# Kernel tuning notes

Measured on AMD Instinct MI355X. Metric: run time of the kernel, lower is better.

## Reference

```python
import jax, jax.numpy as jnp
import numpy as np

B, S, D, H = 4, 2048, 1024, 16
DK = D // H

def setup_inputs() -> dict:
    key = jax.random.key(0)
    ks = jax.random.split(key, 12)
    s = 1.0 / np.sqrt(D)
    return {
        "query": jax.random.normal(ks[0], (B, S, D), jnp.float32),
        "key": jax.random.normal(ks[1], (B, S, D), jnp.float32),
        "value": jax.random.normal(ks[2], (B, S, D), jnp.float32),
        "mask": jax.random.randint(ks[3], (B, S, S), 0, 2, jnp.int32),
        "Wq": jax.random.normal(ks[4], (D, D), jnp.float32) * s,
        "bq": jnp.zeros((D,), jnp.float32),
        "Wk": jax.random.normal(ks[5], (D, D), jnp.float32) * s,
        "bk": jnp.zeros((D,), jnp.float32),
        "Wv": jax.random.normal(ks[6], (D, D), jnp.float32) * s,
        "bv": jnp.zeros((D,), jnp.float32),
        "Wo": jax.random.normal(ks[7], (D, D), jnp.float32) * s,
        "bo": jnp.zeros((D,), jnp.float32),
    }

def _split_heads(x):
    b, s, _ = x.shape
    return x.reshape(b, s, H, DK).transpose(0, 2, 1, 3)  # [b,h,s,dk]

def reference(query, key, value, mask, Wq, bq, Wk, bk, Wv, bv, Wo, bo):
    # torch nn.Linear: y = x @ W.T + b
    Q = _split_heads(query @ Wq.T + bq)
    K = _split_heads(key @ Wk.T + bk)
    V = _split_heads(value @ Wv.T + bv)
    scores = jnp.einsum('bhqd,bhkd->bhqk', Q, K) / np.sqrt(DK)
    scores = jnp.where(mask[:, None, :, :] == 0, jnp.float32(-1e9), scores)
    probs = jax.nn.softmax(scores, axis=-1)
    attn = jnp.einsum('bhqk,bhkd->bhqd', probs, V)
    out = attn.transpose(0, 2, 1, 3).reshape(query.shape[0], -1, H * DK)
    return out @ Wo.T + bo
```

## Files before the change

kernel.cpp:

```cpp
#include <hip/hip_runtime.h>

typedef __attribute__((ext_vector_type(8))) short short8;
typedef __attribute__((ext_vector_type(8))) unsigned short ushort8_t;
typedef __attribute__((ext_vector_type(4))) float floatx4;
typedef __attribute__((ext_vector_type(2))) _Float16 half2_t;
typedef __attribute__((ext_vector_type(4))) _Float16 half4;
typedef __attribute__((ext_vector_type(8))) _Float16 half8;

#define B_ 4
#define S_ 2048
#define D_ 1024
#define H_ 16
#define DK_ 64
#define BS_ (B_ * S_)

union V8u { half8 v8; half4 v4[2]; };
union H16 { _Float16 h; unsigned short u; };

typedef const __attribute__((address_space(1))) void* gvp;
typedef __attribute__((address_space(3))) void* lvp;

static __device__ __forceinline__ unsigned short f2bf(float f) {
  union { float f; unsigned int u; } x; x.f = f;
  unsigned int r = x.u + 0x7fffu + ((x.u >> 16) & 1u);
  return (unsigned short)(r >> 16);
}

static __device__ __forceinline__ half2_t pk_f16(float a, float b) {
  return __builtin_bit_cast(half2_t, __builtin_amdgcn_cvt_pkrtz(a, b));
}

__global__ void cast_kernel(const float* __restrict__ in, unsigned short* __restrict__ out, int n4) {
  int i = blockIdx.x * blockDim.x + threadIdx.x;
  if (i < n4) {
    float4 v = ((const float4*)in)[i];
    ushort4 o;
    o.x = f2bf(v.x); o.y = f2bf(v.y); o.z = f2bf(v.z); o.w = f2bf(v.w);
    ((ushort4*)out)[i] = o;
  }
}

__global__ void cast4_kernel(const float* __restrict__ a, const float* __restrict__ b,
                             const float* __restrict__ c, const float* __restrict__ d,
                             unsigned short* __restrict__ oa, unsigned short* __restrict__ ob,
                             unsigned short* __restrict__ oc, unsigned short* __restrict__ od, int n4) {
  int i = blockIdx.x * blockDim.x + threadIdx.x;
  int w = blockIdx.y;
  const float* src = (w == 0) ? a : (w == 1) ? b : (w == 2) ? c : d;
  unsigned short* dst = (w == 0) ? oa : (w == 1) ? ob : (w == 2) ? oc : od;
  if (i < n4) {
    float4 v = ((const float4*)src)[i];
    ushort4 o;
    o.x = f2bf(v.x); o.y = f2bf(v.y); o.z = f2bf(v.z); o.w = f2bf(v.w);
    ((ushort4*)dst)[i] = o;
  }
}

__global__ void pack_mask(const int* __restrict__ mask, unsigned long long* __restrict__ bits) {
  int i = blockIdx.x * blockDim.x + threadIdx.x;
  unsigned long long m = __ballot(mask[i] != 0);
  if ((threadIdx.x & 63) == 0) bits[i >> 6] = m;
}

__global__ void transpose_v(const unsigned short* __restrict__ Vh, unsigned short* __restrict__ Vt) {
  __shared__ unsigned short T[64][72];
  int bh = blockIdx.y;
  int s0 = blockIdx.x * 64;
  int tid = threadIdx.x;
  int r = tid >> 3, c = (tid & 7) * 8;
  const unsigned short* src = Vh + ((size_t)bh * S_ + s0) * DK_;
#pragma unroll
  for (int p = 0; p < 2; ++p)
    *(uint4*)(&T[r + p * 32][c]) = *(const uint4*)(src + (size_t)(r + p * 32) * DK_ + c);
  __syncthreads();
  unsigned short* dst = Vt + (size_t)bh * DK_ * S_;
#pragma unroll
  for (int p = 0; p < 2; ++p) {
    int d = r + p * 32;
    ushort8_t o;
#pragma unroll
    for (int i = 0; i < 8; ++i) {
      int pos = c + i;
      int th = pos >> 5, rem = pos & 31;
      int q4 = rem >> 3, rem2 = rem & 7;
      int t = th * 2 + (rem2 >> 2), j = rem2 & 3;
      int k = t * 16 + q4 * 4 + j;
      o[i] = T[k][d];
    }
    *(ushort8_t*)(dst + (size_t)d * S_ + s0 + c) = o;
  }
}

__global__ __launch_bounds__(256) void gemm_bt(
    const unsigned short* __restrict__ X,
    const unsigned short* __restrict__ W,
    const float* __restrict__ bias,
    void* __restrict__ Y, int M, int N, int K, float scale, int mode)
{
  __shared__ __align__(16) unsigned short As[128 * 64];
  __shared__ __align__(16) unsigned short Bs[128 * 64];
  int tid = threadIdx.x;
  int wave = tid >> 6, lane = tid & 63, quad = lane >> 4, li = lane & 15;
  int wm = wave >> 1, wn = wave & 1;
  int bm = blockIdx.y, bn = blockIdx.x;

  int srow = lane >> 3;
  int scol = ((lane & 7) ^ srow) * 8;
  const unsigned short* gA = X + (size_t)(bm * 128 + wave * 32 + srow) * K + scol;
  const unsigned short* gB = W + (size_t)(bn * 128 + wave * 32 + srow) * K + scol;
  unsigned short* ldsA = &As[wave * 2048];
  unsigned short* ldsB = &Bs[wave * 2048];

  floatx4 acc[4][4] = {};

  for (int k0 = 0; k0 < K; k0 += 64) {
    __syncthreads();
#pragma unroll
    for (int j = 0; j < 4; ++j) {
      __builtin_amdgcn_global_load_lds((gvp)(gA + (size_t)(j * 8) * K + k0), (lvp)(ldsA + j * 512), 16, 0, 0);
      __builtin_amdgcn_global_load_lds((gvp)(gB + (size_t)(j * 8) * K + k0), (lvp)(ldsB + j * 512), 16, 0, 0);
    }
    __syncthreads();
#pragma unroll
    for (int s2 = 0; s2 < 2; ++s2) {
      short8 af[4], bf[4];
#pragma unroll
      for (int t = 0; t < 4; ++t) {
        int ra = wm * 64 + t * 16 + li;
        int rb = wn * 64 + t * 16 + li;
        int slot = ((s2 * 4 + quad) ^ (li & 7)) * 8;
        af[t] = *(const short8*)(&As[ra * 64 + slot]);
        bf[t] = *(const short8*)(&Bs[rb * 64 + slot]);
      }
#pragma unroll
      for (int mt = 0; mt < 4; ++mt)
#pragma unroll
        for (int nt = 0; nt < 4; ++nt)
          acc[mt][nt] = __builtin_amdgcn_mfma_f32_16x16x32_bf16(af[mt], bf[nt], acc[mt][nt], 0, 0, 0);
    }
  }

#pragma unroll
  for (int nt = 0; nt < 4; ++nt) {
    int n = bn * 128 + wn * 64 + nt * 16 + li;
    float bv = bias[n];
#pragma unroll
    for (int mt = 0; mt < 4; ++mt) {
#pragma unroll
      for (int r = 0; r < 4; ++r) {
        int m = bm * 128 + wm * 64 + mt * 16 + quad * 4 + r;
        float v = (acc[mt][nt][r] + bv) * scale;
        if (mode == 1) {
          ((float*)Y)[(size_t)m * N + n] = v;
        } else {
          int b = m >> 11, s = m & 2047, h = n >> 6, dk = n & 63;
          size_t idx = (((size_t)(b * H_ + h)) * S_ + s) * DK_ + dk;
          if (mode == 0) {
            ((unsigned short*)Y)[idx] = f2bf(v);
          } else {
            H16 hv; hv.h = (_Float16)v;
            ((unsigned short*)Y)[idx] = hv.u;
          }
        }
      }
    }
  }
}

__global__ __launch_bounds__(256) void attn_kernel(
    const unsigned short* __restrict__ Qh,
    const unsigned short* __restrict__ Kh,
    const _Float16* __restrict__ Vt,
    const unsigned long long* __restrict__ mbits,
    unsigned short* __restrict__ attnb)
{
  __shared__ __align__(16) unsigned short Ks[64 * 64];
  __shared__ __align__(16) unsigned short Vs[64 * 64];

  int tid = threadIdx.x;
  int wave = tid >> 6, lane = tid & 63, quad = lane >> 4, li = lane & 15;

  int blk = blockIdx.x;
  int xcd = blk & 7, slot7 = blk >> 3;
  int bh = xcd * 8 + (slot7 >> 4);
  int qb = slot7 & 15;
  int b = bh >> 4, h = bh & 15;
  int qbase = qb * 128 + wave * 32;
  const size_t hq = (size_t)bh * S_ * DK_;

  short8 aQ[2][2];
#pragma unroll
  for (int qs = 0; qs < 2; ++qs)
#pragma unroll
    for (int s2 = 0; s2 < 2; ++s2)
      aQ[qs][s2] = *(const short8*)(Qh + hq + (size_t)(qbase + qs * 16 + li) * DK_ + s2 * 32 + quad * 8);

  floatx4 o[2][4] = {};
  float l[2] = {0.f, 0.f};

  const unsigned long long* mrow = mbits + ((size_t)b * S_ + qbase + li) * (S_ / 64);

  int srow = lane >> 3;
  int scol = ((lane & 7) ^ srow) * 8;
  const unsigned short* gK = Kh + hq + (size_t)(wave * 16 + srow) * DK_ + scol;
  const _Float16* gV = Vt + ((size_t)bh * 64 + wave * 16 + srow) * S_ + scol;
  unsigned short* ldsK = &Ks[(wave * 16) * 64];
  unsigned short* ldsV = &Vs[(wave * 16) * 64];

  for (int k0 = 0; k0 < S_; k0 += 64) {
    int kw = k0 >> 6;
    __syncthreads();
#pragma unroll
    for (int j = 0; j < 2; ++j) {
      __builtin_amdgcn_global_load_lds((gvp)(gK + (size_t)(k0 + j * 8) * DK_), (lvp)(ldsK + j * 512), 16, 0, 0);
      __builtin_amdgcn_global_load_lds((gvp)(gV + (size_t)(j * 8) * S_ + k0), (lvp)(ldsV + j * 512), 16, 0, 0);
    }
    unsigned long long mw0 = mrow[kw];
    unsigned long long mw1 = mrow[16 * (S_ / 64) + kw];
    __syncthreads();

    short8 bK[4][2];
#pragma unroll
    for (int t = 0; t < 4; ++t)
#pragma unroll
      for (int s2 = 0; s2 < 2; ++s2)
        bK[t][s2] = *(const short8*)(&Ks[(t * 16 + li) * 64 + (((s2 * 4 + quad) ^ (li & 7)) * 8)]);

    floatx4 sc[4][2] = {};
#pragma unroll
    for (int s2 = 0; s2 < 2; ++s2)
#pragma unroll
      for (int t = 0; t < 4; ++t)
#pragma unroll
        for (int qs = 0; qs < 2; ++qs)
          sc[t][qs] = __builtin_amdgcn_mfma_f32_16x16x32_bf16(bK[t][s2], aQ[qs][s2], sc[t][qs], 0, 0, 0);

    unsigned long long sh0 = mw0 >> (quad * 4);
    unsigned long long sh1 = mw1 >> (quad * 4);

    half4 aP[4][2];
#pragma unroll
    for (int t = 0; t < 4; ++t)
#pragma unroll
      for (int qs = 0; qs < 2; ++qs) {
        unsigned nb = (unsigned)(((qs ? sh1 : sh0) >> (t * 16)) & 15u);
        float p0 = (nb & 1u)        ? exp2f(sc[t][qs][0]) : 0.f;
        float p1 = ((nb >> 1) & 1u) ? exp2f(sc[t][qs][1]) : 0.f;
        float p2 = ((nb >> 2) & 1u) ? exp2f(sc[t][qs][2]) : 0.f;
        float p3 = ((nb >> 3) & 1u) ? exp2f(sc[t][qs][3]) : 0.f;
        l[qs] += (p0 + p1) + (p2 + p3);
        half2_t plo = pk_f16(p0, p1);
        half2_t phi = pk_f16(p2, p3);
        aP[t][qs] = __builtin_shufflevector(plo, phi, 0, 1, 2, 3);
      }

    V8u vv[4][2];
#pragma unroll
    for (int dt = 0; dt < 4; ++dt)
#pragma unroll
      for (int tp = 0; tp < 2; ++tp)
        vv[dt][tp].v8 = *(const half8*)((const _Float16*)&Vs[(dt * 16 + li) * 64 + (((tp * 4 + quad) ^ (li & 7)) * 8)]);

#pragma unroll
    for (int t = 0; t < 4; ++t)
#pragma unroll
      for (int qs = 0; qs < 2; ++qs)
#pragma unroll
        for (int dt = 0; dt < 4; ++dt)
          o[qs][dt] = __builtin_amdgcn_mfma_f32_16x16x16f16(aP[t][qs], vv[dt][t >> 1].v4[t & 1], o[qs][dt], 0, 0, 0);
  }

  float inv[2];
#pragma unroll
  for (int qs = 0; qs < 2; ++qs) {
    float lf = l[qs];
    lf += __shfl_xor(lf, 16, 64);
    lf += __shfl_xor(lf, 32, 64);
    inv[qs] = 1.0f / lf;
  }
#pragma unroll
  for (int qs = 0; qs < 2; ++qs)
#pragma unroll
    for (int r = 0; r < 4; ++r) {
      float ir = __shfl(inv[qs], quad * 4 + r, 64);
      size_t row = (size_t)b * S_ + qbase + qs * 16 + quad * 4 + r;
#pragma unroll
      for (int dt = 0; dt < 4; ++dt)
        attnb[row * D_ + h * DK_ + dt * 16 + li] = f2bf(o[qs][dt][r] * ir);
    }
}

extern "C" void kernel_launch(void* const* d_in, const int* in_sizes, int n_in,
                              void* d_out, int out_size, void* d_ws, size_t ws_size,
                              hipStream_t stream) {
  const float* query = (const float*)d_in[0];
  const float* key   = (const float*)d_in[1];
  const float* value = (const float*)d_in[2];
  const int*   mask  = (const int*)d_in[3];
  const float* Wq = (const float*)d_in[4];
  const float* bq = (const float*)d_in[5];
  const float* Wk = (const float*)d_in[6];
  const float* bk = (const float*)d_in[7];
  const float* Wv = (const float*)d_in[8];
  const float* bv = (const float*)d_in[9];
  const float* Wo = (const float*)d_in[10];
  const float* bo = (const float*)d_in[11];
  float* out = (float*)d_out;

  char* ws = (char*)d_ws;
  size_t off = 0;
  auto alloc = [&](size_t bytes) -> void* {
    void* p = ws + off;
    off += (bytes + 255) & ~(size_t)255;
    return p;
  };
  unsigned short* Xb    = (unsigned short*)alloc((size_t)BS_ * D_ * 2);
  unsigned short* Wqb   = (unsigned short*)alloc((size_t)D_ * D_ * 2);
  unsigned short* Wkb   = (unsigned short*)alloc((size_t)D_ * D_ * 2);
  unsigned short* Wvb   = (unsigned short*)alloc((size_t)D_ * D_ * 2);
  unsigned short* Wob   = (unsigned short*)alloc((size_t)D_ * D_ * 2);
  unsigned short* Qh    = (unsigned short*)alloc((size_t)BS_ * D_ * 2);
  unsigned short* Kh    = (unsigned short*)alloc((size_t)BS_ * D_ * 2);
  unsigned short* Vh    = (unsigned short*)alloc((size_t)BS_ * D_ * 2);
  unsigned short* Vt    = (unsigned short*)alloc((size_t)BS_ * D_ * 2);
  unsigned short* attnb = (unsigned short*)alloc((size_t)BS_ * D_ * 2);
  unsigned long long* mbits = (unsigned long long*)alloc((size_t)B_ * S_ * (S_ / 64) * 8);

  const float SC = 0.18033688011112042f;

  pack_mask<<<(B_ * S_ * S_) / 256, 256, 0, stream>>>(mask, mbits);

  int wn4 = D_ * D_ / 4;
  cast4_kernel<<<dim3(wn4 / 256, 4), 256, 0, stream>>>(Wq, Wk, Wv, Wo, Wqb, Wkb, Wvb, Wob, wn4);

  int xn4 = BS_ * D_ / 4;
  dim3 gg(D_ / 128, BS_ / 128), gb(256);

  cast_kernel<<<xn4 / 256, 256, 0, stream>>>(query, Xb, xn4);
  gemm_bt<<<gg, gb, 0, stream>>>(Xb, Wqb, bq, Qh, BS_, D_, D_, SC, 0);
  cast_kernel<<<xn4 / 256, 256, 0, stream>>>(key, Xb, xn4);
  gemm_bt<<<gg, gb, 0, stream>>>(Xb, Wkb, bk, Kh, BS_, D_, D_, 1.0f, 0);
  cast_kernel<<<xn4 / 256, 256, 0, stream>>>(value, Xb, xn4);
  gemm_bt<<<gg, gb, 0, stream>>>(Xb, Wvb, bv, Vh, BS_, D_, D_, 1.0f, 2);
  transpose_v<<<dim3(S_ / 64, B_ * H_), 256, 0, stream>>>(Vh, Vt);

  attn_kernel<<<dim3(8 * 8 * 16), 256, 0, stream>>>(Qh, Kh, (const _Float16*)Vt, mbits, attnb);

  gemm_bt<<<gg, gb, 0, stream>>>(attnb, Wob, bo, out, BS_, D_, D_, 1.0f, 1);
}
```

Baseline: 503.4 us.

## Double-buffer GEMM and attention LDS tiles, batch QKV casts and projections

Adds double-buffered shared-memory staging to both the GEMM core and the attention kernel, so the next K/V or A/B tile is prefetched while the current one feeds MFMA, with one barrier per iteration instead of two. The mask words for the next tile are also prefetched. The three input casts and the three QKV projections are merged into single launches over a z-dimension, using separate bf16 buffers. This doubles LDS usage per block, which may reduce occupancy, and uses more workspace memory.

```diff
diff --git a/kernel.cpp b/kernel.cpp
--- a/kernel.cpp
+++ b/kernel.cpp
@@ -30,13 +30,19 @@
   return __builtin_bit_cast(half2_t, __builtin_amdgcn_cvt_pkrtz(a, b));
 }
 
-__global__ void cast_kernel(const float* __restrict__ in, unsigned short* __restrict__ out, int n4) {
+__global__ void cast3_kernel(const float* __restrict__ a, const float* __restrict__ b,
+                             const float* __restrict__ c,
+                             unsigned short* __restrict__ oa, unsigned short* __restrict__ ob,
+                             unsigned short* __restrict__ oc, int n4) {
   int i = blockIdx.x * blockDim.x + threadIdx.x;
+  int w = blockIdx.y;
+  const float* src = (w == 0) ? a : (w == 1) ? b : c;
+  unsigned short* dst = (w == 0) ? oa : (w == 1) ? ob : oc;
   if (i < n4) {
-    float4 v = ((const float4*)in)[i];
+    float4 v = ((const float4*)src)[i];
     ushort4 o;
     o.x = f2bf(v.x); o.y = f2bf(v.y); o.z = f2bf(v.z); o.w = f2bf(v.w);
-    ((ushort4*)out)[i] = o;
+    ((ushort4*)dst)[i] = o;
   }
 }
 
@@ -91,53 +97,54 @@
   }
 }
 
-__global__ __launch_bounds__(256) void gemm_bt(
-    const unsigned short* __restrict__ X,
-    const unsigned short* __restrict__ W,
-    const float* __restrict__ bias,
-    void* __restrict__ Y, int M, int N, int K, float scale, int mode)
+__device__ __forceinline__ void gemm_core(
+    const unsigned short* __restrict__ X, const unsigned short* __restrict__ W,
+    const float* __restrict__ bias, void* __restrict__ Y,
+    float scale, int mode, int bm, int bn,
+    unsigned short* As, unsigned short* Bs)
 {
-  __shared__ __align__(16) unsigned short As[128 * 64];
-  __shared__ __align__(16) unsigned short Bs[128 * 64];
+  constexpr int K = D_, N = D_;
   int tid = threadIdx.x;
   int wave = tid >> 6, lane = tid & 63, quad = lane >> 4, li = lane & 15;
   int wm = wave >> 1, wn = wave & 1;
-  int bm = blockIdx.y, bn = blockIdx.x;
-
   int srow = lane >> 3;
   int scol = ((lane & 7) ^ srow) * 8;
   const unsigned short* gA = X + (size_t)(bm * 128 + wave * 32 + srow) * K + scol;
   const unsigned short* gB = W + (size_t)(bn * 128 + wave * 32 + srow) * K + scol;
-  unsigned short* ldsA = &As[wave * 2048];
-  unsigned short* ldsB = &Bs[wave * 2048];
+
+  auto stage = [&](int buf, int k0) {
+#pragma unroll
+    for (int j = 0; j < 4; ++j) {
+      __builtin_amdgcn_global_load_lds((gvp)(gA + (size_t)(j * 8) * K + k0),
+          (lvp)(As + buf * 8192 + wave * 2048 + j * 512), 16, 0, 0);
+      __builtin_amdgcn_global_load_lds((gvp)(gB + (size_t)(j * 8) * K + k0),
+          (lvp)(Bs + buf * 8192 + wave * 2048 + j * 512), 16, 0, 0);
+    }
+  };
 
   floatx4 acc[4][4] = {};
-
-  for (int k0 = 0; k0 < K; k0 += 64) {
+  stage(0, 0);
+  constexpr int NK = K / 64;
+  for (int i = 0; i < NK; ++i) {
+    int buf = i & 1;
     __syncthreads();
-#pragma unroll
-    for (int j = 0; j < 4; ++j) {
-      __builtin_amdgcn_global_load_lds((gvp)(gA + (size_t)(j * 8) * K + k0), (lvp)(ldsA + j * 512), 16, 0, 0);
-      __builtin_amdgcn_global_load_lds((gvp)(gB + (size_t)(j * 8) * K + k0), (lvp)(ldsB + j * 512), 16, 0, 0);
-    }
-    __syncthreads();
-#pragma unroll
-    for (int s2 = 0; s2 < 2; ++s2) {
-      short8 af[4], bf[4];
+    if (i + 1 < NK) stage(buf ^ 1, (i + 1) * 64);
+    short8 af[2][4], bf[2][4];
+#pragma unroll
+    for (int s2 = 0; s2 < 2; ++s2)
 #pragma unroll
       for (int t = 0; t < 4; ++t) {
-        int ra = wm * 64 + t * 16 + li;
-        int rb = wn * 64 + t * 16 + li;
         int slot = ((s2 * 4 + quad) ^ (li & 7)) * 8;
-        af[t] = *(const short8*)(&As[ra * 64 + slot]);
-        bf[t] = *(const short8*)(&Bs[rb * 64 + slot]);
+        af[s2][t] = *(const short8*)(&As[buf * 8192 + (wm * 64 + t * 16 + li) * 64 + slot]);
+        bf[s2][t] = *(const short8*)(&Bs[buf * 8192 + (wn * 64 + t * 16 + li) * 64 + slot]);
       }
 #pragma unroll
+    for (int s2 = 0; s2 < 2; ++s2)
+#pragma unroll
       for (int mt = 0; mt < 4; ++mt)
 #pragma unroll
         for (int nt = 0; nt < 4; ++nt)
-          acc[mt][nt] = __builtin_amdgcn_mfma_f32_16x16x32_bf16(af[mt], bf[nt], acc[mt][nt], 0, 0, 0);
-    }
+          acc[mt][nt] = __builtin_amdgcn_mfma_f32_16x16x32_bf16(af[s2][mt], bf[s2][nt], acc[mt][nt], 0, 0, 0);
   }
 
 #pragma unroll
@@ -167,6 +174,36 @@
   }
 }
 
+__global__ __launch_bounds__(256) void gemm_qkv(
+    const unsigned short* __restrict__ Xq, const unsigned short* __restrict__ Xk,
+    const unsigned short* __restrict__ Xv,
+    const unsigned short* __restrict__ Wq, const unsigned short* __restrict__ Wk,
+    const unsigned short* __restrict__ Wv,
+    const float* __restrict__ bq, const float* __restrict__ bk, const float* __restrict__ bv,
+    unsigned short* __restrict__ Qh, unsigned short* __restrict__ Kh,
+    unsigned short* __restrict__ Vh, float sc)
+{
+  __shared__ __align__(16) unsigned short As[2 * 8192];
+  __shared__ __align__(16) unsigned short Bs[2 * 8192];
+  int z = blockIdx.z;
+  const unsigned short* X = (z == 0) ? Xq : (z == 1) ? Xk : Xv;
+  const unsigned short* W = (z == 0) ? Wq : (z == 1) ? Wk : Wv;
+  const float* bias = (z == 0) ? bq : (z == 1) ? bk : bv;
+  void* Y = (z == 0) ? (void*)Qh : (z == 1) ? (void*)Kh : (void*)Vh;
+  float scale = (z == 0) ? sc : 1.0f;
+  int mode = (z == 2) ? 2 : 0;
+  gemm_core(X, W, bias, Y, scale, mode, blockIdx.y, blockIdx.x, As, Bs);
+}
+
+__global__ __launch_bounds__(256) void gemm_out(
+    const unsigned short* __restrict__ X, const unsigned short* __restrict__ W,
+    const float* __restrict__ bias, float* __restrict__ Y)
+{
+  __shared__ __align__(16) unsigned short As[2 * 8192];
+  __shared__ __align__(16) unsigned short Bs[2 * 8192];
+  gemm_core(X, W, bias, Y, 1.0f, 1, blockIdx.y, blockIdx.x, As, Bs);
+}
+
 __global__ __launch_bounds__(256) void attn_kernel(
     const unsigned short* __restrict__ Qh,
     const unsigned short* __restrict__ Kh,
@@ -174,8 +211,8 @@
     const unsigned long long* __restrict__ mbits,
     unsigned short* __restrict__ attnb)
 {
-  __shared__ __align__(16) unsigned short Ks[64 * 64];
-  __shared__ __align__(16) unsigned short Vs[64 * 64];
+  __shared__ __align__(16) unsigned short Ks[2 * 4096];
+  __shared__ __align__(16) unsigned short Vs[2 * 4096];
 
   int tid = threadIdx.x;
   int wave = tid >> 6, lane = tid & 63, quad = lane >> 4, li = lane & 15;
@@ -204,27 +241,42 @@
   int scol = ((lane & 7) ^ srow) * 8;
   const unsigned short* gK = Kh + hq + (size_t)(wave * 16 + srow) * DK_ + scol;
   const _Float16* gV = Vt + ((size_t)bh * 64 + wave * 16 + srow) * S_ + scol;
-  unsigned short* ldsK = &Ks[(wave * 16) * 64];
-  unsigned short* ldsV = &Vs[(wave * 16) * 64];
-
-  for (int k0 = 0; k0 < S_; k0 += 64) {
-    int kw = k0 >> 6;
+
+  auto stage = [&](int buf, int k0) {
+#pragma unroll
+    for (int j = 0; j < 2; ++j) {
+      __builtin_amdgcn_global_load_lds((gvp)(gK + (size_t)(k0 + j * 8) * DK_),
+          (lvp)(Ks + buf * 4096 + wave * 1024 + j * 512), 16, 0, 0);
+      __builtin_amdgcn_global_load_lds((gvp)(gV + (size_t)(j * 8) * S_ + k0),
+          (lvp)(Vs + buf * 4096 + wave * 1024 + j * 512), 16, 0, 0);
+    }
+  };
+
+  stage(0, 0);
+  unsigned long long mw0c = mrow[0];
+  unsigned long long mw1c = mrow[16 * (S_ / 64)];
+
+  constexpr int NK = S_ / 64;
+  for (int i = 0; i < NK; ++i) {
+    int buf = i & 1;
     __syncthreads();
-#pragma unroll
-    for (int j = 0; j < 2; ++j) {
-      __builtin_amdgcn_global_load_lds((gvp)(gK + (size_t)(k0 + j * 8) * DK_), (lvp)(ldsK + j * 512), 16, 0, 0);
-      __builtin_amdgcn_global_load_lds((gvp)(gV + (size_t)(j * 8) * S_ + k0), (lvp)(ldsV + j * 512), 16, 0, 0);
-    }
-    unsigned long long mw0 = mrow[kw];
-    unsigned long long mw1 = mrow[16 * (S_ / 64) + kw];
-    __syncthreads();
+    if (i + 1 < NK) stage(buf ^ 1, (i + 1) * 64);
+    unsigned long long mw0n = 0, mw1n = 0;
+    if (i + 1 < NK) { mw0n = mrow[i + 1]; mw1n = mrow[16 * (S_ / 64) + i + 1]; }
 
     short8 bK[4][2];
 #pragma unroll
     for (int t = 0; t < 4; ++t)
 #pragma unroll
       for (int s2 = 0; s2 < 2; ++s2)
-        bK[t][s2] = *(const short8*)(&Ks[(t * 16 + li) * 64 + (((s2 * 4 + quad) ^ (li & 7)) * 8)]);
+        bK[t][s2] = *(const short8*)(&Ks[buf * 4096 + (t * 16 + li) * 64 + (((s2 * 4 + quad) ^ (li & 7)) * 8)]);
+
+    V8u vv[4][2];
+#pragma unroll
+    for (int dt = 0; dt < 4; ++dt)
+#pragma unroll
+      for (int tp = 0; tp < 2; ++tp)
+        vv[dt][tp].v8 = *(const half8*)((const _Float16*)&Vs[buf * 4096 + (dt * 16 + li) * 64 + (((tp * 4 + quad) ^ (li & 7)) * 8)]);
 
     floatx4 sc[4][2] = {};
 #pragma unroll
@@ -235,8 +287,8 @@
         for (int qs = 0; qs < 2; ++qs)
           sc[t][qs] = __builtin_amdgcn_mfma_f32_16x16x32_bf16(bK[t][s2], aQ[qs][s2], sc[t][qs], 0, 0, 0);
 
-    unsigned long long sh0 = mw0 >> (quad * 4);
-    unsigned long long sh1 = mw1 >> (quad * 4);
+    unsigned long long sh0 = mw0c >> (quad * 4);
+    unsigned long long sh1 = mw1c >> (quad * 4);
 
     half4 aP[4][2];
 #pragma unroll
@@ -254,13 +306,6 @@
         aP[t][qs] = __builtin_shufflevector(plo, phi, 0, 1, 2, 3);
       }
 
-    V8u vv[4][2];
-#pragma unroll
-    for (int dt = 0; dt < 4; ++dt)
-#pragma unroll
-      for (int tp = 0; tp < 2; ++tp)
-        vv[dt][tp].v8 = *(const half8*)((const _Float16*)&Vs[(dt * 16 + li) * 64 + (((tp * 4 + quad) ^ (li & 7)) * 8)]);
-
 #pragma unroll
     for (int t = 0; t < 4; ++t)
 #pragma unroll
@@ -268,6 +313,8 @@
 #pragma unroll
         for (int dt = 0; dt < 4; ++dt)
           o[qs][dt] = __builtin_amdgcn_mfma_f32_16x16x16f16(aP[t][qs], vv[dt][t >> 1].v4[t & 1], o[qs][dt], 0, 0, 0);
+
+    mw0c = mw0n; mw1c = mw1n;
   }
 
   float inv[2];
@@ -314,7 +361,9 @@
     off += (bytes + 255) & ~(size_t)255;
     return p;
   };
-  unsigned short* Xb    = (unsigned short*)alloc((size_t)BS_ * D_ * 2);
+  unsigned short* Xq    = (unsigned short*)alloc((size_t)BS_ * D_ * 2);
+  unsigned short* Xk    = (unsigned short*)alloc((size_t)BS_ * D_ * 2);
+  unsigned short* Xv    = (unsigned short*)alloc((size_t)BS_ * D_ * 2);
   unsigned short* Wqb   = (unsigned short*)alloc((size_t)D_ * D_ * 2);
   unsigned short* Wkb   = (unsigned short*)alloc((size_t)D_ * D_ * 2);
   unsigned short* Wvb   = (unsigned short*)alloc((size_t)D_ * D_ * 2);
@@ -334,17 +383,14 @@
   cast4_kernel<<<dim3(wn4 / 256, 4), 256, 0, stream>>>(Wq, Wk, Wv, Wo, Wqb, Wkb, Wvb, Wob, wn4);
 
   int xn4 = BS_ * D_ / 4;
-  dim3 gg(D_ / 128, BS_ / 128), gb(256);
-
-  cast_kernel<<<xn4 / 256, 256, 0, stream>>>(query, Xb, xn4);
-  gemm_bt<<<gg, gb, 0, stream>>>(Xb, Wqb, bq, Qh, BS_, D_, D_, SC, 0);
-  cast_kernel<<<xn4 / 256, 256, 0, stream>>>(key, Xb, xn4);
-  gemm_bt<<<gg, gb, 0, stream>>>(Xb, Wkb, bk, Kh, BS_, D_, D_, 1.0f, 0);
-  cast_kernel<<<xn4 / 256, 256, 0, stream>>>(value, Xb, xn4);
-  gemm_bt<<<gg, gb, 0, stream>>>(Xb, Wvb, bv, Vh, BS_, D_, D_, 1.0f, 2);
+  cast3_kernel<<<dim3(xn4 / 256, 3), 256, 0, stream>>>(query, key, value, Xq, Xk, Xv, xn4);
+
+  gemm_qkv<<<dim3(D_ / 128, BS_ / 128, 3), 256, 0, stream>>>(
+      Xq, Xk, Xv, Wqb, Wkb, Wvb, bq, bk, bv, Qh, Kh, Vh, SC);
+
   transpose_v<<<dim3(S_ / 64, B_ * H_), 256, 0, stream>>>(Vh, Vt);
 
   attn_kernel<<<dim3(8 * 8 * 16), 256, 0, stream>>>(Qh, Kh, (const _Float16*)Vt, mbits, attnb);
 
-  gemm_bt<<<gg, gb, 0, stream>>>(attnb, Wob, bo, out, BS_, D_, D_, 1.0f, 1);
-}
+  gemm_out<<<dim3(D_ / 128, BS_ / 128), 256, 0, stream>>>(attnb, Wob, bo, out);
+}
```

Measured after the change: 503.3 us. No clear change (-0.0%).
